# Performance work log

Hardware: AMD Instinct MI355X
Metric: run time of the kernel (lower is better)

The kernel has to match this reference:

```python
import jax, jax.numpy as jnp
import numpy as np

B, S, E = 2, 2048, 2048
NH, NKV, HD = 16, 4, 128
ROPE_BASE = 10000.0
WINDOW = max(1, S // 2)


def _rotate_half(x):
    x1, x2 = jnp.split(x, 2, axis=-1)
    return jnp.concatenate([-x2, x1], axis=-1)


def setup_inputs() -> dict:
    key = jax.random.key(0)
    ks = jax.random.split(key, 6)
    x = jax.random.normal(ks[0], (B, S, E), dtype=jnp.float32)
    Wq = jax.random.normal(ks[1], (NH * HD, E), dtype=jnp.float32) * 0.02
    Wk = jax.random.normal(ks[2], (NKV * HD, E), dtype=jnp.float32) * 0.02
    Wv = jax.random.normal(ks[3], (NKV * HD, E), dtype=jnp.float32) * 0.02
    Wo = jax.random.normal(ks[4], (E, E), dtype=jnp.float32) * 0.02
    # RoPE tables, duplicated-half layout matching _rotate_half
    inv_freq = 1.0 / (ROPE_BASE ** (jnp.arange(0, HD, 2, dtype=jnp.float32) / HD))
    angles = jnp.arange(S, dtype=jnp.float32)[:, None] * inv_freq[None, :]  # [S, HD/2]
    emb = jnp.concatenate([angles, angles], axis=-1)  # [S, HD]
    cos = jnp.cos(emb)[:, None, :]  # [S, 1, HD] -> broadcasts over heads
    sin = jnp.sin(emb)[:, None, :]
    return {"x": x, "cos": cos, "sin": sin, "Wq": Wq, "Wk": Wk, "Wv": Wv, "Wo": Wo}


def reference(x, cos, sin, Wq, Wk, Wv, Wo):
    b, s, _ = x.shape
    q = (x @ Wq.T).reshape(b, s, NH, HD)
    k = (x @ Wk.T).reshape(b, s, NKV, HD)
    v = (x @ Wv.T).reshape(b, s, NKV, HD)
    # rotary (cos/sin broadcast [S,1,HD] over batch/heads)
    q = q * cos + _rotate_half(q) * sin
    k = k * cos + _rotate_half(k) * sin
    # GQA expand: repeat_interleave over head dim
    factor = NH // NKV
    k = jnp.repeat(k, factor, axis=2)  # [b,s,NH,HD]
    v = jnp.repeat(v, factor, axis=2)
    # local causal mask: 0 <= (i - j) < window
    pos = jnp.arange(s)
    dist = pos[:, None] - pos[None, :]
    mask = (dist >= 0) & (dist < WINDOW)  # [S,S]
    scale = 1.0 / jnp.sqrt(jnp.asarray(HD, dtype=x.dtype))
    scores = jnp.einsum("bqhd,bkhd->bhqk", q, k) * scale
    scores = jnp.where(mask[None, None, :, :], scores, jnp.asarray(-1e30, dtype=scores.dtype))
    attn = jax.nn.softmax(scores, axis=-1)
    out = jnp.einsum("bhqk,bkhd->bqhd", attn, v)
    out = out.reshape(b, s, NH * HD)
    return out @ Wo.T
```

## Files before the change

### kernel.cpp

```cpp
#include <hip/hip_runtime.h>

#define S_LEN 2048
#define EMB 2048
#define NH 16
#define NKV 4
#define HD 128
#define WINDOW 1024
#define BATCH 2

typedef _Float16 half8 __attribute__((ext_vector_type(8)));
typedef _Float16 half4 __attribute__((ext_vector_type(4)));
typedef float f32x4 __attribute__((ext_vector_type(4)));

#define MFMA16(a, b, c) __builtin_amdgcn_mfma_f32_16x16x32_f16((a), (b), (c), 0, 0, 0)

__device__ __forceinline__ void gload16(const void* g, void* l) {
  __builtin_amdgcn_global_load_lds(
      (const __attribute__((address_space(1))) unsigned int*)g,
      (__attribute__((address_space(3))) unsigned int*)l, 16, 0, 0);
}

__global__ __launch_bounds__(256)
void convert_all(const float* __restrict__ x, const float* __restrict__ wq,
                 const float* __restrict__ wk, const float* __restrict__ wv,
                 const float* __restrict__ wo, _Float16* __restrict__ dst) {
  size_t i = (size_t)blockIdx.x * 256 + threadIdx.x;
  const float* src; size_t u; size_t dbase;
  if (i < 1048576)      { src = x;  u = i;           dbase = 0; }
  else if (i < 1572864) { src = wq; u = i - 1048576; dbase = 8388608; }
  else if (i < 1703936) { src = wk; u = i - 1572864; dbase = 12582912; }
  else if (i < 1835008) { src = wv; u = i - 1703936; dbase = 13631488; }
  else                  { src = wo; u = i - 1835008; dbase = 14680064; }
  f32x4 a = *(const f32x4*)(src + u * 8);
  f32x4 b = *(const f32x4*)(src + u * 8 + 4);
  half8 h = { (_Float16)a[0], (_Float16)a[1], (_Float16)a[2], (_Float16)a[3],
              (_Float16)b[0], (_Float16)b[1], (_Float16)b[2], (_Float16)b[3] };
  *(half8*)(dst + dbase + u * 8) = h;
}

__global__ __launch_bounds__(256)
void qkv_gemm(const _Float16* __restrict__ x16, const _Float16* __restrict__ Wq16,
              const _Float16* __restrict__ Wk16, const _Float16* __restrict__ Wv16,
              _Float16* __restrict__ Qh, _Float16* __restrict__ Kr,
              _Float16* __restrict__ Vt) {
  __shared__ _Float16 Asm[2][128 * 32];
  __shared__ _Float16 Bsm[2][128 * 32];
  const int K = EMB;
  int m0 = blockIdx.y * 128, n0 = blockIdx.x * 128;
  const _Float16* Wp; int c0, sel;
  if (n0 < 2048)      { Wp = Wq16; c0 = n0;        sel = 0; }
  else if (n0 < 2560) { Wp = Wk16; c0 = n0 - 2048; sel = 1; }
  else                { Wp = Wv16; c0 = n0 - 2560; sel = 2; }

  int t = threadIdx.x, lane = t & 63, w = t >> 6;
  int l15 = lane & 15, quad = lane >> 4;
  int wm = (w >> 1) * 64, wn = (w & 1) * 64;

  auto stage = [&](int kt, int p) {
#pragma unroll
    for (int i = 0; i < 2; ++i) {
      int u = t + 256 * i;
      int row = u >> 2, cc = u & 3, g = cc ^ (row & 3);
      gload16(x16 + (size_t)(m0 + row) * K + kt + g * 8, (char*)Asm[p] + (size_t)u * 16);
      gload16(Wp + (size_t)(c0 + row) * K + kt + g * 8, (char*)Bsm[p] + (size_t)u * 16);
    }
  };

  f32x4 acc[4][4] = {};
  stage(0, 0);
  for (int it = 0; it < 64; ++it) {
    int p = it & 1;
    __syncthreads();
    if (it < 63) stage((it + 1) * 32, 1 - p);
    half8 af[4], bf[4];
#pragma unroll
    for (int i = 0; i < 4; ++i) {
      int row = wm + i * 16 + l15;
      af[i] = *(const half8*)&Asm[p][row * 32 + ((quad ^ (row & 3)) << 3)];
    }
#pragma unroll
    for (int i = 0; i < 4; ++i) {
      int row = wn + i * 16 + l15;
      bf[i] = *(const half8*)&Bsm[p][row * 32 + ((quad ^ (row & 3)) << 3)];
    }
#pragma unroll
    for (int mi = 0; mi < 4; ++mi)
#pragma unroll
      for (int ni = 0; ni < 4; ++ni)
        acc[mi][ni] = MFMA16(af[mi], bf[ni], acc[mi][ni]);
  }
#pragma unroll
  for (int mi = 0; mi < 4; ++mi)
#pragma unroll
    for (int ni = 0; ni < 4; ++ni)
#pragma unroll
      for (int r = 0; r < 4; ++r) {
        int row = m0 + wm + mi * 16 + quad * 4 + r;
        int col = c0 + wn + ni * 16 + l15;
        _Float16 val = (_Float16)acc[mi][ni][r];
        if (sel == 0) {
          Qh[(size_t)row * 2048 + col] = val;
        } else {
          int b = row >> 11, s = row & 2047, kvh = col >> 7, d = col & 127;
          if (sel == 1)
            Kr[((size_t)(b * NKV + kvh) * S_LEN + s) * HD + d] = val;
          else
            Vt[((size_t)(b * NKV + kvh) * HD + d) * S_LEN + s] = val;
        }
      }
}

__global__ __launch_bounds__(256)
void rope_k(_Float16* __restrict__ Kr, const float* __restrict__ cosT,
            const float* __restrict__ sinT) {
  int t = threadIdx.x;
  int row = blockIdx.x * 32 + (t >> 3);
  int s = row & (S_LEN - 1);
  int d0 = (t & 7) * 8;
  _Float16* p = Kr + (size_t)row * HD;
  half8 lo = *(half8*)(p + d0);
  half8 hi = *(half8*)(p + d0 + 64);
  float cv[8], sv[8];
  *(f32x4*)&cv[0] = *(const f32x4*)(cosT + (size_t)s * HD + d0);
  *(f32x4*)&cv[4] = *(const f32x4*)(cosT + (size_t)s * HD + d0 + 4);
  *(f32x4*)&sv[0] = *(const f32x4*)(sinT + (size_t)s * HD + d0);
  *(f32x4*)&sv[4] = *(const f32x4*)(sinT + (size_t)s * HD + d0 + 4);
  half8 rlo, rhi;
#pragma unroll
  for (int u = 0; u < 8; ++u) {
    float l = (float)lo[u], h = (float)hi[u];
    rlo[u] = (_Float16)(l * cv[u] - h * sv[u]);
    rhi[u] = (_Float16)(h * cv[u] + l * sv[u]);
  }
  *(half8*)(p + d0) = rlo;
  *(half8*)(p + d0 + 64) = rhi;
}

__global__ __launch_bounds__(256, 2)
void attn_fused(const _Float16* Qh, const _Float16* __restrict__ Kr,
                const _Float16* __restrict__ Vt, const float* __restrict__ cosT,
                const float* __restrict__ sinT, _Float16* Oh) {
  const float SL2E = 0.08838834764831843f * 1.4426950408889634f;
  int c = blockIdx.x & 255, half = blockIdx.x >> 8;
  int h = c & 15, j = c >> 4;
  int qt = half ? (15 - j) : j;
  int b = half;
  int kvh = h >> 2;
  int q0 = qt * 128;
  int t = threadIdx.x, lane = t & 63, w = t >> 6;
  int l15 = lane & 15, quad = lane >> 4;

  __shared__ _Float16 Ksm[2][64 * 128];
  __shared__ _Float16 Vsm[2][128 * 64];
  __shared__ _Float16 PB[4][2][2][64 * 8];

  int qw0 = q0 + w * 32;

  half8 qf[2][4];
#pragma unroll
  for (int g = 0; g < 2; ++g) {
    int qi = qw0 + g * 16 + l15;
    const _Float16* qrow = Qh + (size_t)(b * S_LEN + qi) * EMB + h * HD;
    const float* crow = cosT + (size_t)qi * HD;
    const float* srow = sinT + (size_t)qi * HD;
    float qv[4][8], cv[2][8], sv[2][8];
#pragma unroll
    for (int kc = 0; kc < 4; ++kc) {
      half8 q8 = *(const half8*)(qrow + kc * 32 + quad * 8);
#pragma unroll
      for (int jj = 0; jj < 8; ++jj) qv[kc][jj] = (float)q8[jj];
    }
#pragma unroll
    for (int kc = 0; kc < 2; ++kc) {
      int d0 = kc * 32 + quad * 8;
      *(f32x4*)&cv[kc][0] = *(const f32x4*)(crow + d0);
      *(f32x4*)&cv[kc][4] = *(const f32x4*)(crow + d0 + 4);
      *(f32x4*)&sv[kc][0] = *(const f32x4*)(srow + d0);
      *(f32x4*)&sv[kc][4] = *(const f32x4*)(srow + d0 + 4);
    }
#pragma unroll
    for (int kc = 0; kc < 4; ++kc)
#pragma unroll
      for (int jj = 0; jj < 8; ++jj) {
        float rot = (kc < 2) ? -qv[kc + 2][jj] : qv[kc - 2][jj];
        qf[g][kc][jj] = (_Float16)((qv[kc][jj] * cv[kc & 1][jj] + rot * sv[kc & 1][jj]) * SL2E);
      }
  }

  const _Float16* khead = Kr + (size_t)(b * NKV + kvh) * S_LEN * HD;
  const _Float16* vhead = Vt + (size_t)(b * NKV + kvh) * HD * S_LEN;

  auto stage = [&](int kt, int p) {
    int k0 = kt * 64;
#pragma unroll
    for (int i = 0; i < 4; ++i) {
      int u = t + 256 * i;
      int r = u >> 4, cc = u & 15;
      gload16(khead + (((size_t)(k0 + r)) << 7) + ((cc ^ (r & 15)) << 3),
              (char*)Ksm[p] + (size_t)u * 16);
    }
#pragma unroll
    for (int i = 0; i < 4; ++i) {
      int u = t + 256 * i;
      int d = u >> 3, cc = u & 7;
      gload16(vhead + (((size_t)d) << 11) + k0 + ((cc ^ (d & 7)) << 3),
              (char*)Vsm[p] + (size_t)u * 16);
    }
  };

  f32x4 oacc[2][8] = {};
  float l_r[2] = {0.f, 0.f};

  int kt_lo = (q0 >= WINDOW) ? ((q0 - (WINDOW - 1)) >> 6) : 0;
  int kt_hi = qt * 2 + 1;

  stage(kt_lo, 0);
  for (int kt = kt_lo; kt <= kt_hi; ++kt) {
    int p = (kt - kt_lo) & 1;
    int k0 = kt * 64;
    __syncthreads();
    if (kt < kt_hi) stage(kt + 1, 1 - p);

    f32x4 sfr[2][4];
#pragma unroll
    for (int nb = 0; nb < 4; ++nb) {
      int r = nb * 16 + l15;
      half8 kf[4];
#pragma unroll
      for (int dc = 0; dc < 4; ++dc) {
        int cw = dc * 4 + quad;
        kf[dc] = *(const half8*)&Ksm[p][r * 128 + ((cw ^ l15) << 3)];
      }
      f32x4 s0 = {0.f, 0.f, 0.f, 0.f}, s1 = {0.f, 0.f, 0.f, 0.f};
#pragma unroll
      for (int dc = 0; dc < 4; ++dc) {
        s0 = MFMA16(kf[dc], qf[0][dc], s0);
        s1 = MFMA16(kf[dc], qf[1][dc], s1);
      }
      sfr[0][nb] = s0; sfr[1][nb] = s1;
    }

#pragma unroll
    for (int g = 0; g < 2; ++g) {
      int qi = qw0 + g * 16 + l15;
#pragma unroll
      for (int nb = 0; nb < 4; ++nb) {
        half4 ph;
#pragma unroll
        for (int r = 0; r < 4; ++r) {
          int key = k0 + nb * 16 + quad * 4 + r;
          int dd = qi - key;
          float sv = (dd >= 0 && dd < WINDOW) ? sfr[g][nb][r] : -1e4f;
          float pv = __builtin_amdgcn_exp2f(fminf(sv, 14.0f));
          l_r[g] += pv;
          ph[r] = (_Float16)pv;
        }
        *(half4*)&PB[w][g][nb >> 1]
            [((l15 + 16 * (((nb & 1) << 1) + (quad >> 1))) << 3) + ((quad & 1) << 2)] = ph;
      }
    }

    half8 pf[2][2];
#pragma unroll
    for (int g = 0; g < 2; ++g) {
      pf[g][0] = *(const half8*)&PB[w][g][0][lane << 3];
      pf[g][1] = *(const half8*)&PB[w][g][1][lane << 3];
    }

#pragma unroll
    for (int nc = 0; nc < 8; ++nc) {
      int d = nc * 16 + l15;
      half8 v0 = *(const half8*)&Vsm[p][d * 64 + ((quad ^ (d & 7)) << 3)];
      half8 v1 = *(const half8*)&Vsm[p][d * 64 + (((4 + quad) ^ (d & 7)) << 3)];
      oacc[0][nc] = MFMA16(v0, pf[0][0], oacc[0][nc]);
      oacc[0][nc] = MFMA16(v1, pf[0][1], oacc[0][nc]);
      oacc[1][nc] = MFMA16(v0, pf[1][0], oacc[1][nc]);
      oacc[1][nc] = MFMA16(v1, pf[1][1], oacc[1][nc]);
    }
  }

#pragma unroll
  for (int g = 0; g < 2; ++g) {
    float lr = l_r[g];
    lr += __shfl_xor(lr, 16, 64);
    lr += __shfl_xor(lr, 32, 64);
    float inv = 1.0f / lr;
    int qi = qw0 + g * 16 + l15;
    _Float16* orow = Oh + (size_t)(b * S_LEN + qi) * EMB + h * HD;
#pragma unroll
    for (int nc = 0; nc < 8; ++nc) {
      half4 o4;
#pragma unroll
      for (int r = 0; r < 4; ++r) o4[r] = (_Float16)(oacc[g][nc][r] * inv);
      *(half4*)&orow[nc * 16 + quad * 4] = o4;
    }
  }
}

__global__ __launch_bounds__(256)
void out_gemm(const _Float16* __restrict__ A, const _Float16* __restrict__ B,
              float* __restrict__ out) {
  __shared__ _Float16 Asm[2][128 * 32];
  __shared__ _Float16 Bsm[2][128 * 32];
  const int K = EMB;
  int m0 = blockIdx.y * 128, n0 = blockIdx.x * 128;
  int t = threadIdx.x, lane = t & 63, w = t >> 6;
  int l15 = lane & 15, quad = lane >> 4;
  int wm = (w >> 1) * 64, wn = (w & 1) * 64;

  auto stage = [&](int kt, int p) {
#pragma unroll
    for (int i = 0; i < 2; ++i) {
      int u = t + 256 * i;
      int row = u >> 2, cc = u & 3, g = cc ^ (row & 3);
      gload16(A + (size_t)(m0 + row) * K + kt + g * 8, (char*)Asm[p] + (size_t)u * 16);
      gload16(B + (size_t)(n0 + row) * K + kt + g * 8, (char*)Bsm[p] + (size_t)u * 16);
    }
  };

  f32x4 acc[4][4] = {};
  stage(0, 0);
  for (int it = 0; it < 64; ++it) {
    int p = it & 1;
    __syncthreads();
    if (it < 63) stage((it + 1) * 32, 1 - p);
    half8 af[4], bf[4];
#pragma unroll
    for (int i = 0; i < 4; ++i) {
      int row = wm + i * 16 + l15;
      af[i] = *(const half8*)&Asm[p][row * 32 + ((quad ^ (row & 3)) << 3)];
    }
#pragma unroll
    for (int i = 0; i < 4; ++i) {
      int row = wn + i * 16 + l15;
      bf[i] = *(const half8*)&Bsm[p][row * 32 + ((quad ^ (row & 3)) << 3)];
    }
#pragma unroll
    for (int mi = 0; mi < 4; ++mi)
#pragma unroll
      for (int ni = 0; ni < 4; ++ni)
        acc[mi][ni] = MFMA16(af[mi], bf[ni], acc[mi][ni]);
  }
#pragma unroll
  for (int mi = 0; mi < 4; ++mi)
#pragma unroll
    for (int ni = 0; ni < 4; ++ni)
#pragma unroll
      for (int r = 0; r < 4; ++r) {
        int row = m0 + wm + mi * 16 + quad * 4 + r;
        int col = n0 + wn + ni * 16 + l15;
        out[(size_t)row * EMB + col] = acc[mi][ni][r];
      }
}

extern "C" void kernel_launch(void* const* d_in, const int* in_sizes, int n_in,
                              void* d_out, int out_size, void* d_ws, size_t ws_size,
                              hipStream_t stream) {
  const float* x    = (const float*)d_in[0];
  const float* cosT = (const float*)d_in[1];
  const float* sinT = (const float*)d_in[2];
  const float* Wq   = (const float*)d_in[3];
  const float* Wk   = (const float*)d_in[4];
  const float* Wv   = (const float*)d_in[5];
  const float* Wo   = (const float*)d_in[6];
  float* out = (float*)d_out;

  char* ws = (char*)d_ws;
  _Float16* x16  = (_Float16*)(ws);
  _Float16* Wq16 = (_Float16*)(ws + 16777216);
  _Float16* Wk16 = (_Float16*)(ws + 25165824);
  _Float16* Wv16 = (_Float16*)(ws + 27262976);
  _Float16* Wo16 = (_Float16*)(ws + 29360128);
  _Float16* Qh   = (_Float16*)(ws + 37748736);
  _Float16* Kr   = (_Float16*)(ws + 54525952);
  _Float16* Vt   = (_Float16*)(ws + 58720256);
  _Float16* Oh   = Qh;

  convert_all<<<dim3(9216), 256, 0, stream>>>(x, Wq, Wk, Wv, Wo, (_Float16*)ws);
  qkv_gemm<<<dim3(24, 32), 256, 0, stream>>>(x16, Wq16, Wk16, Wv16, Qh, Kr, Vt);
  rope_k<<<dim3(512), 256, 0, stream>>>(Kr, cosT, sinT);
  attn_fused<<<dim3(512), 256, 0, stream>>>(Qh, Kr, Vt, cosT, sinT, Oh);
  out_gemm<<<dim3(16, 32), 256, 0, stream>>>(Oh, Wo16, out);
}
```

Measured before the change: 303.5 us.

## Stage GEMM tiles through registers with BK=64 and vectorize V-transpose store

```diff
diff --git a/kernel.cpp b/kernel.cpp
--- a/kernel.cpp
+++ b/kernel.cpp
@@ -43,8 +43,8 @@
               const _Float16* __restrict__ Wk16, const _Float16* __restrict__ Wv16,
               _Float16* __restrict__ Qh, _Float16* __restrict__ Kr,
               _Float16* __restrict__ Vt) {
-  __shared__ _Float16 Asm[2][128 * 32];
-  __shared__ _Float16 Bsm[2][128 * 32];
+  __shared__ _Float16 Asm[128 * 64];
+  __shared__ _Float16 Bsm[128 * 64];
   const int K = EMB;
   int m0 = blockIdx.y * 128, n0 = blockIdx.x * 128;
   const _Float16* Wp; int c0, sel;
@@ -56,58 +56,74 @@
   int l15 = lane & 15, quad = lane >> 4;
   int wm = (w >> 1) * 64, wn = (w & 1) * 64;
 
-  auto stage = [&](int kt, int p) {
-#pragma unroll
-    for (int i = 0; i < 2; ++i) {
-      int u = t + 256 * i;
-      int row = u >> 2, cc = u & 3, g = cc ^ (row & 3);
-      gload16(x16 + (size_t)(m0 + row) * K + kt + g * 8, (char*)Asm[p] + (size_t)u * 16);
-      gload16(Wp + (size_t)(c0 + row) * K + kt + g * 8, (char*)Bsm[p] + (size_t)u * 16);
+  int srow = t >> 3, sc = t & 7;
+  int gc = sc ^ (srow & 7);
+  const _Float16* agp = x16 + (size_t)(m0 + srow) * K + gc * 8;
+  const _Float16* bgp = Wp + (size_t)(c0 + srow) * K + gc * 8;
+
+  half8 ar[4], br[4];
+  auto gload = [&](int kt) {
+#pragma unroll
+    for (int p = 0; p < 4; ++p) {
+      ar[p] = *(const half8*)(agp + (size_t)p * 32 * K + kt);
+      br[p] = *(const half8*)(bgp + (size_t)p * 32 * K + kt);
     }
   };
 
   f32x4 acc[4][4] = {};
-  stage(0, 0);
-  for (int it = 0; it < 64; ++it) {
-    int p = it & 1;
+  gload(0);
+  for (int it = 0; it < 32; ++it) {
     __syncthreads();
-    if (it < 63) stage((it + 1) * 32, 1 - p);
-    half8 af[4], bf[4];
-#pragma unroll
-    for (int i = 0; i < 4; ++i) {
-      int row = wm + i * 16 + l15;
-      af[i] = *(const half8*)&Asm[p][row * 32 + ((quad ^ (row & 3)) << 3)];
-    }
-#pragma unroll
-    for (int i = 0; i < 4; ++i) {
-      int row = wn + i * 16 + l15;
-      bf[i] = *(const half8*)&Bsm[p][row * 32 + ((quad ^ (row & 3)) << 3)];
-    }
-#pragma unroll
-    for (int mi = 0; mi < 4; ++mi)
-#pragma unroll
-      for (int ni = 0; ni < 4; ++ni)
-        acc[mi][ni] = MFMA16(af[mi], bf[ni], acc[mi][ni]);
+#pragma unroll
+    for (int p = 0; p < 4; ++p) {
+      *(half8*)((char*)Asm + p * 4096 + t * 16) = ar[p];
+      *(half8*)((char*)Bsm + p * 4096 + t * 16) = br[p];
+    }
+    __syncthreads();
+    if (it < 31) gload((it + 1) * 64);
+#pragma unroll
+    for (int kc = 0; kc < 2; ++kc) {
+      half8 af[4], bf[4];
+#pragma unroll
+      for (int i = 0; i < 4; ++i) {
+        int row = wm + i * 16 + l15;
+        af[i] = *(const half8*)&Asm[row * 64 + (((kc * 4 + quad) ^ (row & 7)) * 8)];
+      }
+#pragma unroll
+      for (int i = 0; i < 4; ++i) {
+        int row = wn + i * 16 + l15;
+        bf[i] = *(const half8*)&Bsm[row * 64 + (((kc * 4 + quad) ^ (row & 7)) * 8)];
+      }
+#pragma unroll
+      for (int mi = 0; mi < 4; ++mi)
+#pragma unroll
+        for (int ni = 0; ni < 4; ++ni)
+          acc[mi][ni] = MFMA16(af[mi], bf[ni], acc[mi][ni]);
+    }
   }
 #pragma unroll
   for (int mi = 0; mi < 4; ++mi)
 #pragma unroll
-    for (int ni = 0; ni < 4; ++ni)
-#pragma unroll
-      for (int r = 0; r < 4; ++r) {
-        int row = m0 + wm + mi * 16 + quad * 4 + r;
-        int col = c0 + wn + ni * 16 + l15;
-        _Float16 val = (_Float16)acc[mi][ni][r];
-        if (sel == 0) {
-          Qh[(size_t)row * 2048 + col] = val;
-        } else {
-          int b = row >> 11, s = row & 2047, kvh = col >> 7, d = col & 127;
-          if (sel == 1)
-            Kr[((size_t)(b * NKV + kvh) * S_LEN + s) * HD + d] = val;
-          else
-            Vt[((size_t)(b * NKV + kvh) * HD + d) * S_LEN + s] = val;
-        }
-      }
+    for (int ni = 0; ni < 4; ++ni) {
+      int row0 = m0 + wm + mi * 16 + quad * 4;
+      int col = c0 + wn + ni * 16 + l15;
+      if (sel == 0) {
+#pragma unroll
+        for (int r = 0; r < 4; ++r)
+          Qh[(size_t)(row0 + r) * 2048 + col] = (_Float16)acc[mi][ni][r];
+      } else if (sel == 1) {
+        int b = row0 >> 11, s = row0 & 2047, kvh = col >> 7, d = col & 127;
+#pragma unroll
+        for (int r = 0; r < 4; ++r)
+          Kr[((size_t)(b * NKV + kvh) * S_LEN + s + r) * HD + d] = (_Float16)acc[mi][ni][r];
+      } else {
+        int b = row0 >> 11, s = row0 & 2047, kvh = col >> 7, d = col & 127;
+        half4 v4;
+#pragma unroll
+        for (int r = 0; r < 4; ++r) v4[r] = (_Float16)acc[mi][ni][r];
+        *(half4*)&Vt[((size_t)(b * NKV + kvh) * HD + d) * S_LEN + s] = v4;
+      }
+    }
 }
 
 __global__ __launch_bounds__(256)
@@ -300,46 +316,58 @@
 __global__ __launch_bounds__(256)
 void out_gemm(const _Float16* __restrict__ A, const _Float16* __restrict__ B,
               float* __restrict__ out) {
-  __shared__ _Float16 Asm[2][128 * 32];
-  __shared__ _Float16 Bsm[2][128 * 32];
+  __shared__ _Float16 Asm[128 * 64];
+  __shared__ _Float16 Bsm[128 * 64];
   const int K = EMB;
   int m0 = blockIdx.y * 128, n0 = blockIdx.x * 128;
   int t = threadIdx.x, lane = t & 63, w = t >> 6;
   int l15 = lane & 15, quad = lane >> 4;
   int wm = (w >> 1) * 64, wn = (w & 1) * 64;
 
-  auto stage = [&](int kt, int p) {
-#pragma unroll
-    for (int i = 0; i < 2; ++i) {
-      int u = t + 256 * i;
-      int row = u >> 2, cc = u & 3, g = cc ^ (row & 3);
-      gload16(A + (size_t)(m0 + row) * K + kt + g * 8, (char*)Asm[p] + (size_t)u * 16);
-      gload16(B + (size_t)(n0 + row) * K + kt + g * 8, (char*)Bsm[p] + (size_t)u * 16);
+  int srow = t >> 3, sc = t & 7;
+  int gc = sc ^ (srow & 7);
+  const _Float16* agp = A + (size_t)(m0 + srow) * K + gc * 8;
+  const _Float16* bgp = B + (size_t)(n0 + srow) * K + gc * 8;
+
+  half8 ar[4], br[4];
+  auto gload = [&](int kt) {
+#pragma unroll
+    for (int p = 0; p < 4; ++p) {
+      ar[p] = *(const half8*)(agp + (size_t)p * 32 * K + kt);
+      br[p] = *(const half8*)(bgp + (size_t)p * 32 * K + kt);
     }
   };
 
   f32x4 acc[4][4] = {};
-  stage(0, 0);
-  for (int it = 0; it < 64; ++it) {
-    int p = it & 1;
+  gload(0);
+  for (int it = 0; it < 32; ++it) {
     __syncthreads();
-    if (it < 63) stage((it + 1) * 32, 1 - p);
-    half8 af[4], bf[4];
-#pragma unroll
-    for (int i = 0; i < 4; ++i) {
-      int row = wm + i * 16 + l15;
-      af[i] = *(const half8*)&Asm[p][row * 32 + ((quad ^ (row & 3)) << 3)];
-    }
-#pragma unroll
-    for (int i = 0; i < 4; ++i) {
-      int row = wn + i * 16 + l15;
-      bf[i] = *(const half8*)&Bsm[p][row * 32 + ((quad ^ (row & 3)) << 3)];
-    }
-#pragma unroll
-    for (int mi = 0; mi < 4; ++mi)
-#pragma unroll
-      for (int ni = 0; ni < 4; ++ni)
-        acc[mi][ni] = MFMA16(af[mi], bf[ni], acc[mi][ni]);
+#pragma unroll
+    for (int p = 0; p < 4; ++p) {
+      *(half8*)((char*)Asm + p * 4096 + t * 16) = ar[p];
+      *(half8*)((char*)Bsm + p * 4096 + t * 16) = br[p];
+    }
+    __syncthreads();
+    if (it < 31) gload((it + 1) * 64);
+#pragma unroll
+    for (int kc = 0; kc < 2; ++kc) {
+      half8 af[4], bf[4];
+#pragma unroll
+      for (int i = 0; i < 4; ++i) {
+        int row = wm + i * 16 + l15;
+        af[i] = *(const half8*)&Asm[row * 64 + (((kc * 4 + quad) ^ (row & 7)) * 8)];
+      }
+#pragma unroll
+      for (int i = 0; i < 4; ++i) {
+        int row = wn + i * 16 + l15;
+        bf[i] = *(const half8*)&Bsm[row * 64 + (((kc * 4 + quad) ^ (row & 7)) * 8)];
+      }
+#pragma unroll
+      for (int mi = 0; mi < 4; ++mi)
+#pragma unroll
+        for (int ni = 0; ni < 4; ++ni)
+          acc[mi][ni] = MFMA16(af[mi], bf[ni], acc[mi][ni]);
+    }
   }
 #pragma unroll
   for (int mi = 0; mi < 4; ++mi)
```

Result: faster. 278.8 us (-8.2%).
